# Optimization experiments

Hardware: AMD Instinct MI355X
Metric: run time of the kernel (lower is better)

The kernel has to match this reference:

```python
import jax, jax.numpy as jnp
from jax import lax
import numpy as np

B, L, D, HS, T, N = 1024, 96, 128, 512, 24, 128  # batch, former_seq_len, input_dim, hidden_dim, output_dim, temp_node


def setup_inputs() -> dict:
    key = jax.random.key(0)
    ks = jax.random.split(key, 14)
    s = 1.0 / np.sqrt(HS)  # init std used by the torch module
    f32 = jnp.float32
    return {
        "H": jax.random.normal(ks[0], (B, L, D), f32),
        "y_0": jax.random.normal(ks[1], (B, 1), f32),
        "embedding": jax.random.normal(ks[2], (B, 2 * HS), f32),
        "Y": jax.random.normal(ks[3], (B, T), f32),
        "Wa": jax.random.normal(ks[4], (D, T, N), f32) * s,
        "Ua": jax.random.normal(ks[5], (HS, T, N), f32) * s,
        "ba": jax.random.normal(ks[6], (T, N), f32) * s,
        "Va": jax.random.normal(ks[7], (N, T, 1), f32) * s,
        "W": jax.random.normal(ks[8], (D, T, 4 * HS), f32) * s,
        "U": jax.random.normal(ks[9], (HS, T, 4 * HS), f32) * s,
        "bias": jax.random.normal(ks[10], (T, 4 * HS), f32) * s,
        "W_y": jax.random.normal(ks[11], (1, T, 4 * HS), f32) * s,
        "fc_w": jax.random.normal(ks[12], (T, HS), f32) * s,  # output_fc[t].weight (row vec)
        "fc_b": jax.random.normal(ks[13], (T,), f32) * s,      # output_fc[t].bias
        "epoch": 3,
    }


def reference(H, y_0, embedding, Y, Wa, Ua, ba, Va, W, U, bias, W_y, fc_w, fc_b, epoch):
    scale = 1.0 / jnp.sqrt(jnp.asarray(HS, H.dtype))
    h0 = embedding[:, :HS]
    c0 = embedding[:, HS:]

    # time-major parameter stacks for lax.scan
    xs = (
        jnp.transpose(Wa, (1, 0, 2)),   # [T, D, N]
        jnp.transpose(Ua, (1, 0, 2)),   # [T, HS, N]
        ba,                              # [T, N]
        jnp.transpose(Va, (1, 0, 2)),   # [T, N, 1]
        jnp.transpose(W, (1, 0, 2)),    # [T, D, 4HS]
        jnp.transpose(U, (1, 0, 2)),    # [T, HS, 4HS]
        bias,                            # [T, 4HS]
        jnp.transpose(W_y, (1, 0, 2)),  # [T, 1, 4HS]
        fc_w,                            # [T, HS]
        fc_b,                            # [T]
    )

    def step(carry, p):
        h_l, c_l, y_prev = carry  # [B,HS], [B,HS], [B,1]
        wa, ua, ba_t, va, w, u, b, wy, fw, fb = p
        # temporal attention over the encoder history
        e = jnp.tanh(jnp.einsum('bld,dn->bln', H, wa) + (c_l @ ua)[:, None, :] + ba_t)  # [B,L,N]
        score = jnp.einsum('bln,n->bl', e, va[:, 0]) * scale                              # [B,L]
        beta = jax.nn.softmax(score, axis=1)
        h_t = jnp.einsum('bl,bld->bd', beta, H)                                           # [B,D]
        # 4-gate LSTM update with teacher-signal injection
        gates = h_t @ w + h_l @ u + b + y_prev @ wy                                       # [B,4HS]
        i = jax.nn.sigmoid(gates[:, :HS])
        f = jax.nn.sigmoid(gates[:, HS:2 * HS])
        g = jnp.tanh(gates[:, 2 * HS:3 * HS])
        o = jax.nn.sigmoid(gates[:, 3 * HS:])
        c_new = f * c_l + i * g
        h_new = o * jnp.tanh(c_new)
        y = h_new @ fw + fb                                                               # [B]
        return (h_new, c_new, y[:, None]), (y, h_new)

    _, (ys, hs) = lax.scan(step, (h0, c0, y_0), xs)
    y_out = ys.T                           # [B, T]
    hidden_seq = jnp.transpose(hs, (1, 0, 2))  # [B, T, HS]
    return y_out, hidden_seq
```

## Files before the change

kernel.cpp:

```cpp
#include <hip/hip_runtime.h>
#include <math.h>

constexpr int NB  = 1024;
constexpr int NL  = 96;
constexpr int ND  = 128;
constexpr int NHS = 512;
constexpr int NT  = 24;
constexpr int NN  = 128;
constexpr int NG4 = 4 * NHS;
constexpr int NK  = ND + NHS;
constexpr int BL  = NB * NL;

typedef __attribute__((ext_vector_type(8))) short bf16x8;
typedef __attribute__((ext_vector_type(4))) float f32x4;

static __device__ __forceinline__ unsigned short f2b(float x) {
    union { float f; unsigned u; } v; v.f = x;
    unsigned r = v.u + 0x7fffu + ((v.u >> 16) & 1u);
    return (unsigned short)(r >> 16);
}
static __device__ __forceinline__ float b2f(unsigned short s) {
    union { unsigned u; float f; } v; v.u = ((unsigned)s) << 16;
    return v.f;
}

constexpr float LOG2E  = 1.4426950408889634f;
static __device__ __forceinline__ float fast_exp(float x) {
    return __builtin_amdgcn_exp2f(x * LOG2E);
}
static __device__ __forceinline__ float fast_tanh(float x) {
    float e2 = __builtin_amdgcn_exp2f(x * (2.0f * LOG2E));
    return 1.0f - 2.0f * __builtin_amdgcn_rcpf(1.0f + e2);
}
static __device__ __forceinline__ float fast_sigmoid(float x) {
    float e = __builtin_amdgcn_exp2f(-x * LOG2E);
    return __builtin_amdgcn_rcpf(1.0f + e);
}

__global__ __launch_bounds__(256) void k_init(const float* __restrict__ emb,
                                              const float* __restrict__ y0,
                                              float* __restrict__ c,
                                              unsigned short* __restrict__ Ab0,
                                              float* __restrict__ y) {
    int idx = blockIdx.x * blockDim.x + threadIdx.x;
    if (idx < NB * NHS) {
        int b = idx / NHS, s = idx - b * NHS;
        Ab0[(size_t)b * NK + ND + s] = f2b(emb[b * 2 * NHS + s]);
        c[idx] = emb[b * 2 * NHS + NHS + s];
    }
    if (idx < NB) y[idx] = y0[idx];
}

__global__ __launch_bounds__(256) void k_prep(const float* __restrict__ H,
                                              unsigned short* __restrict__ Hbf) {
    int idx = (blockIdx.x * 256 + threadIdx.x) * 8;
    float4 a = *(const float4*)(H + idx);
    float4 b = *(const float4*)(H + idx + 4);
    bf16x8 o;
    o[0] = (short)f2b(a.x); o[1] = (short)f2b(a.y);
    o[2] = (short)f2b(a.z); o[3] = (short)f2b(a.w);
    o[4] = (short)f2b(b.x); o[5] = (short)f2b(b.y);
    o[6] = (short)f2b(b.z); o[7] = (short)f2b(b.w);
    *(bf16x8*)(Hbf + idx) = o;
}

__global__ __launch_bounds__(128) void k_prepwa(const float* __restrict__ Wa,
                                                unsigned short* __restrict__ Wab) {
    int tn = blockIdx.x;
    int t = tn / NN, n = tn - t * NN;
    int d = threadIdx.x;
    Wab[(size_t)tn * ND + d] = f2b(Wa[(size_t)d * (NT * NN) + t * NN + n]);
}

__global__ __launch_bounds__(256) void k_prepw(const float* __restrict__ W,
                                               const float* __restrict__ U,
                                               unsigned short* __restrict__ Wg) {
    __shared__ unsigned short ts[64][66];
    int nc = blockIdx.x;
    int kc = blockIdx.y;
    int t  = blockIdx.z;
    int tid = threadIdx.x;
    int rowt = tid >> 4;
    int n4   = (tid & 15) << 2;
#pragma unroll
    for (int i = 0; i < 4; ++i) {
        int kl = i * 16 + rowt;
        int k  = kc * 64 + kl;
        const float* src = (k < ND) ? (W + (size_t)k * (NT * NG4))
                                    : (U + (size_t)(k - ND) * (NT * NG4));
        float4 v = *(const float4*)&src[t * NG4 + nc * 64 + n4];
        ts[kl][n4 + 0] = f2b(v.x);
        ts[kl][n4 + 1] = f2b(v.y);
        ts[kl][n4 + 2] = f2b(v.z);
        ts[kl][n4 + 3] = f2b(v.w);
    }
    __syncthreads();
    size_t base = (((size_t)t * 10 + kc) * NG4 + nc * 64) * 64;
#pragma unroll
    for (int p = 0; p < 2; ++p) {
        int flat = p * 256 + tid;
        int nl = flat >> 3, k8 = (flat & 7) << 3;
        bf16x8 o;
#pragma unroll
        for (int j = 0; j < 8; ++j) o[j] = (short)ts[k8 + j][nl];
        *(bf16x8*)&Wg[base + (size_t)nl * 64 + k8] = o;
    }
}

__global__ __launch_bounds__(256) void k_cua0(const float* __restrict__ c,
                                              const float* __restrict__ Ua,
                                              float* __restrict__ cua_part) {
    __shared__ float cs[16][132];
    int m0 = blockIdx.x * 16, n0 = blockIdx.y;
    int tid = threadIdx.x;
#pragma unroll
    for (int i = 0; i < 8; ++i) {
        int idx = tid + i * 256;
        int row = idx >> 7, k = idx & 127;
        cs[row][k] = c[(size_t)(m0 + row) * NHS + n0 * 128 + k];
    }
    __syncthreads();
    int n = tid & 127, rg = tid >> 7;
    float a8[8] = {0, 0, 0, 0, 0, 0, 0, 0};
    for (int k = 0; k < 128; ++k) {
        float ua = Ua[(size_t)(n0 * 128 + k) * (NT * NN) + n];
#pragma unroll
        for (int i = 0; i < 8; ++i) a8[i] += cs[rg * 8 + i][k] * ua;
    }
#pragma unroll
    for (int i = 0; i < 8; ++i)
        cua_part[((size_t)(m0 + rg * 8 + i) * 4 + n0) * 128 + n] = a8[i];
}

__global__ __launch_bounds__(384, 2) void k_attn_fused(
        const unsigned short* __restrict__ Hbf,
        const unsigned short* __restrict__ Wab,
        const float* __restrict__ Va,
        const float* __restrict__ ba,
        const float* __restrict__ cua_part,
        const float* __restrict__ fcb,
        const float* __restrict__ y_part,
        float* __restrict__ y_st,
        float* __restrict__ out_y,
        unsigned short* __restrict__ Ab,
        int t) {
    __shared__ unsigned short Ws[NN][136];
    __shared__ float sc[NL];
    __shared__ float cua_s[NN];
    __shared__ float red[24][ND];
    int tid = threadIdx.x;
    int b = blockIdx.x;

    const unsigned short* src = Wab + (size_t)t * NN * ND;
    for (int f = tid; f < 2048; f += 384) {
        int n = f >> 4, d0 = (f & 15) << 3;
        *(bf16x8*)&Ws[n][d0] = *(const bf16x8*)(src + n * ND + d0);
    }
    if (tid < 128) {
        const float* cp = cua_part + (size_t)b * 4 * 128 + tid;
        cua_s[tid] = cp[0] + cp[128] + cp[256] + cp[384] + ba[t * NN + tid];
    }
    if (t > 0 && tid == 383) {
        const float* yp = y_part + b * 4;
        float yv = fcb[t - 1] + yp[0] + yp[1] + yp[2] + yp[3];
        y_st[b] = yv;
        out_y[b * NT + (t - 1)] = yv;
    }
    __syncthreads();

    int lane = tid & 63, wave = tid >> 6;
    int ln = lane & 15, kg = lane >> 4;
    const unsigned short* Hrow = Hbf + ((size_t)b * NL + wave * 16 + ln) * ND;

    f32x4 zero = {0.f, 0.f, 0.f, 0.f};
    f32x4 acc[8];
#pragma unroll
    for (int nt = 0; nt < 8; ++nt) acc[nt] = zero;
#pragma unroll
    for (int kc = 0; kc < 4; ++kc) {
        int d0 = kc * 32 + kg * 8;
        bf16x8 a = *(const bf16x8*)(Hrow + d0);
#pragma unroll
        for (int nt = 0; nt < 8; ++nt) {
            bf16x8 bb = *(const bf16x8*)&Ws[nt * 16 + ln][d0];
            acc[nt] = __builtin_amdgcn_mfma_f32_16x16x32_bf16(a, bb, acc[nt], 0, 0, 0);
        }
    }
    float va_l[8];
#pragma unroll
    for (int nt = 0; nt < 8; ++nt) va_l[nt] = Va[(nt * 16 + ln) * NT + t];
    const float scale = 0.044194173824159216f;
#pragma unroll
    for (int r = 0; r < 4; ++r) {
        float s = 0.f;
#pragma unroll
        for (int nt = 0; nt < 8; ++nt) {
            float pre = acc[nt][r] + cua_s[nt * 16 + ln];
            s += va_l[nt] * fast_tanh(pre);
        }
#pragma unroll
        for (int off = 1; off < 16; off <<= 1) s += __shfl_xor(s, off);
        if (ln == 0) sc[wave * 16 + kg * 4 + r] = s * scale;
    }
    __syncthreads();

    if (tid < 64) {
        float s0 = sc[tid];
        float s1 = (tid < 32) ? sc[64 + tid] : -1e30f;
        float m = fmaxf(s0, s1);
#pragma unroll
        for (int off = 32; off; off >>= 1) m = fmaxf(m, __shfl_xor(m, off));
        float p0 = fast_exp(s0 - m);
        float p1 = (tid < 32) ? fast_exp(s1 - m) : 0.f;
        float ssum = p0 + p1;
#pragma unroll
        for (int off = 32; off; off >>= 1) ssum += __shfl_xor(ssum, off);
        float inv = __builtin_amdgcn_rcpf(ssum);
        sc[tid] = p0 * inv;
        if (tid < 32) sc[64 + tid] = p1 * inv;
    }
    __syncthreads();

    int dc = tid & 15, lg = tid >> 4;
    int d0 = dc * 8;
    const unsigned short* Hb = Hbf + (size_t)b * NL * ND;
    float a8[8] = {0, 0, 0, 0, 0, 0, 0, 0};
#pragma unroll
    for (int i = 0; i < 4; ++i) {
        int l = lg * 4 + i;
        bf16x8 hv = *(const bf16x8*)(Hb + l * ND + d0);
        float w = sc[l];
#pragma unroll
        for (int j = 0; j < 8; ++j) a8[j] += w * b2f((unsigned short)hv[j]);
    }
#pragma unroll
    for (int j = 0; j < 8; ++j) red[lg][d0 + j] = a8[j];
    __syncthreads();
    if (tid < ND) {
        float accd = 0.f;
#pragma unroll
        for (int g = 0; g < 24; ++g) accd += red[g][tid];
        Ab[(size_t)b * NK + tid] = f2b(accd);
    }
}

__global__ __launch_bounds__(256, 2) void k_gates_cell(
        const unsigned short* __restrict__ Ab,
        unsigned short* __restrict__ AbN,
        const unsigned short* __restrict__ Wg,
        const float* __restrict__ bias,
        const float* __restrict__ Wy,
        const float* __restrict__ fcw,
        const float* __restrict__ Ua,
        const float* __restrict__ y_st,
        float* __restrict__ c,
        float* __restrict__ out_h,
        float* __restrict__ y_part,
        float* __restrict__ cua_part,
        int t) {
    __shared__ __align__(16) char pool[73728];
    __shared__ float ys[16];
    __shared__ float yredL[16][2];
    int tid = threadIdx.x;
    int lane = tid & 63, wave = tid >> 6;
    int ln = lane & 15, kg = lane >> 4;
    int m0 = blockIdx.x * 16, n0 = blockIdx.y;

    if (tid < 16) ys[tid] = y_st[m0 + tid];

    unsigned short* BstW = (unsigned short*)pool + wave * (128 * 72);
    const unsigned short* Arow = Ab + (size_t)(m0 + ln) * NK;

    f32x4 zero = {0.f, 0.f, 0.f, 0.f};
    f32x4 acc[8];
#pragma unroll
    for (int nt = 0; nt < 8; ++nt) acc[nt] = zero;

    for (int kb = 0; kb < 10; ++kb) {
        const unsigned short* Wkb = Wg
            + (((size_t)(t * 10 + kb)) * NG4 + wave * NHS + n0 * 128) * 64;
#pragma unroll
        for (int i = 0; i < 16; ++i) {
            int flat = i * 64 + lane;
            int n = flat >> 3, k8 = (flat & 7) << 3;
            *(bf16x8*)&BstW[n * 72 + k8] = *(const bf16x8*)(Wkb + (size_t)n * 64 + k8);
        }
#pragma unroll
        for (int kc = 0; kc < 2; ++kc) {
            int d0 = kc * 32 + kg * 8;
            bf16x8 a = *(const bf16x8*)(Arow + kb * 64 + d0);
#pragma unroll
            for (int nt = 0; nt < 8; ++nt) {
                bf16x8 bb = *(const bf16x8*)&BstW[(nt * 16 + ln) * 72 + d0];
                acc[nt] = __builtin_amdgcn_mfma_f32_16x16x32_bf16(a, bb, acc[nt], 0, 0, 0);
            }
        }
    }
    __syncthreads();

    float* gs = (float*)pool;
    float* cs = (float*)(pool + 33792);
#pragma unroll
    for (int nt = 0; nt < 8; ++nt)
#pragma unroll
        for (int r = 0; r < 4; ++r)
            gs[wave * 2112 + (kg * 4 + r) * 132 + nt * 16 + ln] = acc[nt][r];
    __syncthreads();

    int s_loc = tid & 127, rg = tid >> 7;
    int s_glob = n0 * 128 + s_loc;
    float prow[8];
#pragma unroll
    for (int i = 0; i < 8; ++i) {
        int row = rg * 8 + i;
        int b = m0 + row;
        float yp = ys[row];
        float gi = gs[0 * 2112 + row * 132 + s_loc] + bias[t * NG4 + s_glob]
                 + yp * Wy[t * NG4 + s_glob];
        float gf = gs[1 * 2112 + row * 132 + s_loc] + bias[t * NG4 + NHS + s_glob]
                 + yp * Wy[t * NG4 + NHS + s_glob];
        float gg = gs[2 * 2112 + row * 132 + s_loc] + bias[t * NG4 + 2 * NHS + s_glob]
                 + yp * Wy[t * NG4 + 2 * NHS + s_glob];
        float go = gs[3 * 2112 + row * 132 + s_loc] + bias[t * NG4 + 3 * NHS + s_glob]
                 + yp * Wy[t * NG4 + 3 * NHS + s_glob];
        float iv = fast_sigmoid(gi);
        float fv = fast_sigmoid(gf);
        float gv = fast_tanh(gg);
        float ov = fast_sigmoid(go);
        float cn = fv * c[(size_t)b * NHS + s_glob] + iv * gv;
        float hn = ov * fast_tanh(cn);
        c[(size_t)b * NHS + s_glob] = cn;
        cs[row * 132 + s_loc] = cn;
        AbN[(size_t)b * NK + ND + s_glob] = f2b(hn);
        out_h[(size_t)b * (NT * NHS) + t * NHS + s_glob] = hn;
        prow[i] = hn * fcw[t * NHS + s_glob];
    }
#pragma unroll
    for (int i = 0; i < 8; ++i) {
        float v = prow[i];
#pragma unroll
        for (int off = 32; off; off >>= 1) v += __shfl_xor(v, off);
        if (lane == 0) yredL[rg * 8 + i][(tid >> 6) & 1] = v;
    }
    __syncthreads();
    if (tid < 16)
        y_part[(size_t)(m0 + tid) * 4 + n0] = yredL[tid][0] + yredL[tid][1];

    if (t + 1 < NT) {
        float a8[8] = {0, 0, 0, 0, 0, 0, 0, 0};
        int n = s_loc;
        for (int k = 0; k < 128; ++k) {
            float ua = Ua[(size_t)(n0 * 128 + k) * (NT * NN) + (t + 1) * NN + n];
#pragma unroll
            for (int i = 0; i < 8; ++i) a8[i] += cs[(rg * 8 + i) * 132 + k] * ua;
        }
#pragma unroll
        for (int i = 0; i < 8; ++i)
            cua_part[((size_t)(m0 + rg * 8 + i) * 4 + n0) * 128 + n] = a8[i];
    }
}

__global__ __launch_bounds__(256) void k_yfin(const float* __restrict__ y_part,
                                              const float* __restrict__ fcb,
                                              float* __restrict__ out_y) {
    int b = blockIdx.x * 256 + threadIdx.x;
    if (b < NB) {
        const float* yp = y_part + (size_t)b * 4;
        out_y[b * NT + (NT - 1)] = fcb[NT - 1] + yp[0] + yp[1] + yp[2] + yp[3];
    }
}

extern "C" void kernel_launch(void* const* d_in, const int* in_sizes, int n_in,
                              void* d_out, int out_size, void* d_ws, size_t ws_size,
                              hipStream_t stream) {
    (void)in_sizes; (void)n_in; (void)out_size; (void)ws_size;
    const float* H    = (const float*)d_in[0];
    const float* y0   = (const float*)d_in[1];
    const float* emb  = (const float*)d_in[2];
    const float* Wa   = (const float*)d_in[4];
    const float* Ua   = (const float*)d_in[5];
    const float* ba   = (const float*)d_in[6];
    const float* Va   = (const float*)d_in[7];
    const float* W    = (const float*)d_in[8];
    const float* U    = (const float*)d_in[9];
    const float* bias = (const float*)d_in[10];
    const float* Wy   = (const float*)d_in[11];
    const float* fcw  = (const float*)d_in[12];
    const float* fcb  = (const float*)d_in[13];

    float* out_y = (float*)d_out;
    float* out_h = out_y + NB * NT;

    float* ws       = (float*)d_ws;
    float* c_st     = ws;
    float* y_st     = c_st + NB * NHS;
    float* y_part   = y_st + NB;
    float* cua_part = y_part + NB * 4;
    unsigned short* Hbf = (unsigned short*)(cua_part + NB * 4 * 128);
    unsigned short* Wab = Hbf + (size_t)BL * ND;
    unsigned short* Ab0 = Wab + (size_t)NT * NN * ND;
    unsigned short* Ab1 = Ab0 + (size_t)NB * NK;
    unsigned short* Wg  = Ab1 + (size_t)NB * NK;

    hipLaunchKernelGGL(k_init, dim3((NB * NHS) / 256), dim3(256), 0, stream,
                       emb, y0, c_st, Ab0, y_st);
    hipLaunchKernelGGL(k_prep, dim3(BL * ND / (256 * 8)), dim3(256), 0, stream, H, Hbf);
    hipLaunchKernelGGL(k_prepwa, dim3(NT * NN), dim3(128), 0, stream, Wa, Wab);
    hipLaunchKernelGGL(k_prepw, dim3(32, 10, 24), dim3(256), 0, stream, W, U, Wg);
    hipLaunchKernelGGL(k_cua0, dim3(64, 4), dim3(256), 0, stream, c_st, Ua, cua_part);

    for (int t = 0; t < NT; ++t) {
        unsigned short* Ab  = (t & 1) ? Ab1 : Ab0;
        unsigned short* AbN = (t & 1) ? Ab0 : Ab1;
        hipLaunchKernelGGL(k_attn_fused, dim3(NB), dim3(384), 0, stream,
                           Hbf, Wab, Va, ba, cua_part, fcb, y_part, y_st, out_y, Ab, t);
        hipLaunchKernelGGL(k_gates_cell, dim3(64, 4), dim3(256), 0, stream,
                           Ab, AbN, Wg, bias, Wy, fcw, Ua, y_st, c_st,
                           out_h, y_part, cua_part, t);
    }
    hipLaunchKernelGGL(k_yfin, dim3(NB / 256), dim3(256), 0, stream, y_part, fcb, out_y);
}
```

Before: 1.365 ms.

## Fuse per-timestep attention and LSTM kernels into one persistent cooperative kernel

Replaces the 48 per-timestep kernel launches (attention plus gates/cell) and the final y kernel with a single cooperative persistent kernel of 256 blocks × 512 threads that loops over timesteps and uses grid-wide syncs between phases. Each block now handles 4 batch rows for attention and a 16×128 gate tile. The aim is to remove launch overhead and inter-kernel gaps. In exchange it adds grid barrier cost, lowers parallelism (256 blocks versus 1024 for attention), and changes the weighted-sum loop to a scalar per-element form.

```diff
diff --git a/kernel.cpp b/kernel.cpp
--- a/kernel.cpp
+++ b/kernel.cpp
@@ -1,5 +1,8 @@
 #include <hip/hip_runtime.h>
+#include <hip/hip_cooperative_groups.h>
 #include <math.h>
+
+namespace cg = cooperative_groups;
 
 constexpr int NB  = 1024;
 constexpr int NL  = 96;
@@ -132,239 +135,234 @@
         cua_part[((size_t)(m0 + rg * 8 + i) * 4 + n0) * 128 + n] = a8[i];
 }
 
-__global__ __launch_bounds__(384, 2) void k_attn_fused(
+__global__ __launch_bounds__(512, 2) void k_seq(
         const unsigned short* __restrict__ Hbf,
         const unsigned short* __restrict__ Wab,
         const float* __restrict__ Va,
         const float* __restrict__ ba,
-        const float* __restrict__ cua_part,
-        const float* __restrict__ fcb,
-        const float* __restrict__ y_part,
-        float* __restrict__ y_st,
-        float* __restrict__ out_y,
-        unsigned short* __restrict__ Ab,
-        int t) {
-    __shared__ unsigned short Ws[NN][136];
-    __shared__ float sc[NL];
-    __shared__ float cua_s[NN];
-    __shared__ float red[24][ND];
-    int tid = threadIdx.x;
-    int b = blockIdx.x;
-
-    const unsigned short* src = Wab + (size_t)t * NN * ND;
-    for (int f = tid; f < 2048; f += 384) {
-        int n = f >> 4, d0 = (f & 15) << 3;
-        *(bf16x8*)&Ws[n][d0] = *(const bf16x8*)(src + n * ND + d0);
-    }
-    if (tid < 128) {
-        const float* cp = cua_part + (size_t)b * 4 * 128 + tid;
-        cua_s[tid] = cp[0] + cp[128] + cp[256] + cp[384] + ba[t * NN + tid];
-    }
-    if (t > 0 && tid == 383) {
-        const float* yp = y_part + b * 4;
-        float yv = fcb[t - 1] + yp[0] + yp[1] + yp[2] + yp[3];
-        y_st[b] = yv;
-        out_y[b * NT + (t - 1)] = yv;
-    }
-    __syncthreads();
-
-    int lane = tid & 63, wave = tid >> 6;
-    int ln = lane & 15, kg = lane >> 4;
-    const unsigned short* Hrow = Hbf + ((size_t)b * NL + wave * 16 + ln) * ND;
-
-    f32x4 zero = {0.f, 0.f, 0.f, 0.f};
-    f32x4 acc[8];
-#pragma unroll
-    for (int nt = 0; nt < 8; ++nt) acc[nt] = zero;
-#pragma unroll
-    for (int kc = 0; kc < 4; ++kc) {
-        int d0 = kc * 32 + kg * 8;
-        bf16x8 a = *(const bf16x8*)(Hrow + d0);
-#pragma unroll
-        for (int nt = 0; nt < 8; ++nt) {
-            bf16x8 bb = *(const bf16x8*)&Ws[nt * 16 + ln][d0];
-            acc[nt] = __builtin_amdgcn_mfma_f32_16x16x32_bf16(a, bb, acc[nt], 0, 0, 0);
-        }
-    }
-    float va_l[8];
-#pragma unroll
-    for (int nt = 0; nt < 8; ++nt) va_l[nt] = Va[(nt * 16 + ln) * NT + t];
-    const float scale = 0.044194173824159216f;
-#pragma unroll
-    for (int r = 0; r < 4; ++r) {
-        float s = 0.f;
-#pragma unroll
-        for (int nt = 0; nt < 8; ++nt) {
-            float pre = acc[nt][r] + cua_s[nt * 16 + ln];
-            s += va_l[nt] * fast_tanh(pre);
-        }
-#pragma unroll
-        for (int off = 1; off < 16; off <<= 1) s += __shfl_xor(s, off);
-        if (ln == 0) sc[wave * 16 + kg * 4 + r] = s * scale;
-    }
-    __syncthreads();
-
-    if (tid < 64) {
-        float s0 = sc[tid];
-        float s1 = (tid < 32) ? sc[64 + tid] : -1e30f;
-        float m = fmaxf(s0, s1);
-#pragma unroll
-        for (int off = 32; off; off >>= 1) m = fmaxf(m, __shfl_xor(m, off));
-        float p0 = fast_exp(s0 - m);
-        float p1 = (tid < 32) ? fast_exp(s1 - m) : 0.f;
-        float ssum = p0 + p1;
-#pragma unroll
-        for (int off = 32; off; off >>= 1) ssum += __shfl_xor(ssum, off);
-        float inv = __builtin_amdgcn_rcpf(ssum);
-        sc[tid] = p0 * inv;
-        if (tid < 32) sc[64 + tid] = p1 * inv;
-    }
-    __syncthreads();
-
-    int dc = tid & 15, lg = tid >> 4;
-    int d0 = dc * 8;
-    const unsigned short* Hb = Hbf + (size_t)b * NL * ND;
-    float a8[8] = {0, 0, 0, 0, 0, 0, 0, 0};
-#pragma unroll
-    for (int i = 0; i < 4; ++i) {
-        int l = lg * 4 + i;
-        bf16x8 hv = *(const bf16x8*)(Hb + l * ND + d0);
-        float w = sc[l];
-#pragma unroll
-        for (int j = 0; j < 8; ++j) a8[j] += w * b2f((unsigned short)hv[j]);
-    }
-#pragma unroll
-    for (int j = 0; j < 8; ++j) red[lg][d0 + j] = a8[j];
-    __syncthreads();
-    if (tid < ND) {
-        float accd = 0.f;
-#pragma unroll
-        for (int g = 0; g < 24; ++g) accd += red[g][tid];
-        Ab[(size_t)b * NK + tid] = f2b(accd);
-    }
-}
-
-__global__ __launch_bounds__(256, 2) void k_gates_cell(
-        const unsigned short* __restrict__ Ab,
-        unsigned short* __restrict__ AbN,
-        const unsigned short* __restrict__ Wg,
         const float* __restrict__ bias,
         const float* __restrict__ Wy,
         const float* __restrict__ fcw,
+        const float* __restrict__ fcb,
         const float* __restrict__ Ua,
-        const float* __restrict__ y_st,
+        const unsigned short* __restrict__ Wg,
         float* __restrict__ c,
-        float* __restrict__ out_h,
+        float* __restrict__ y_st,
         float* __restrict__ y_part,
         float* __restrict__ cua_part,
-        int t) {
+        unsigned short* __restrict__ Ab0,
+        unsigned short* __restrict__ Ab1,
+        float* __restrict__ out_y,
+        float* __restrict__ out_h) {
+    cg::grid_group gg = cg::this_grid();
     __shared__ __align__(16) char pool[73728];
-    __shared__ float ys[16];
+    __shared__ float sc4[4][NL];
+    __shared__ float cua_s4[4][NN];
     __shared__ float yredL[16][2];
+
+    int blk = blockIdx.x;
     int tid = threadIdx.x;
     int lane = tid & 63, wave = tid >> 6;
     int ln = lane & 15, kg = lane >> 4;
-    int m0 = blockIdx.x * 16, n0 = blockIdx.y;
-
-    if (tid < 16) ys[tid] = y_st[m0 + tid];
-
-    unsigned short* BstW = (unsigned short*)pool + wave * (128 * 72);
-    const unsigned short* Arow = Ab + (size_t)(m0 + ln) * NK;
-
+    int b0 = blk * 4;
+    const float scale_c = 0.044194173824159216f;
     f32x4 zero = {0.f, 0.f, 0.f, 0.f};
-    f32x4 acc[8];
-#pragma unroll
-    for (int nt = 0; nt < 8; ++nt) acc[nt] = zero;
-
-    for (int kb = 0; kb < 10; ++kb) {
-        const unsigned short* Wkb = Wg
-            + (((size_t)(t * 10 + kb)) * NG4 + wave * NHS + n0 * 128) * 64;
-#pragma unroll
-        for (int i = 0; i < 16; ++i) {
-            int flat = i * 64 + lane;
-            int n = flat >> 3, k8 = (flat & 7) << 3;
-            *(bf16x8*)&BstW[n * 72 + k8] = *(const bf16x8*)(Wkb + (size_t)n * 64 + k8);
+
+    for (int t = 0; t < NT; ++t) {
+        unsigned short* AbC = (t & 1) ? Ab1 : Ab0;
+        unsigned short* AbN = (t & 1) ? Ab0 : Ab1;
+
+        {
+            unsigned short* Ws = (unsigned short*)pool;
+            const unsigned short* src = Wab + (size_t)t * NN * ND;
+#pragma unroll
+            for (int f = 0; f < 4; ++f) {
+                int idx = tid + f * 512;
+                int n = idx >> 4, d0 = (idx & 15) << 3;
+                *(bf16x8*)&Ws[n * 136 + d0] = *(const bf16x8*)(src + n * ND + d0);
+            }
+            {
+                int bl = tid >> 7, n = tid & 127;
+                const float* cp = cua_part + (size_t)(b0 + bl) * 512 + n;
+                cua_s4[bl][n] = cp[0] + cp[128] + cp[256] + cp[384] + ba[t * NN + n];
+            }
+            if (t > 0 && tid < 4) {
+                int b = b0 + tid;
+                const float* yp = y_part + (size_t)b * 4;
+                float yv = fcb[t - 1] + yp[0] + yp[1] + yp[2] + yp[3];
+                y_st[b] = yv;
+                out_y[b * NT + (t - 1)] = yv;
+            }
+            __syncthreads();
+
+            float va_l[8];
+#pragma unroll
+            for (int nt = 0; nt < 8; ++nt) va_l[nt] = Va[(nt * 16 + ln) * NT + t];
+
+#pragma unroll
+            for (int ti = 0; ti < 3; ++ti) {
+                int tau = wave + ti * 8;
+                int bl = tau / 6, r0 = (tau % 6) * 16;
+                const unsigned short* Hrow = Hbf + ((size_t)(b0 + bl) * NL + r0 + ln) * ND;
+                f32x4 acc[8];
+#pragma unroll
+                for (int nt = 0; nt < 8; ++nt) acc[nt] = zero;
+#pragma unroll
+                for (int kc = 0; kc < 4; ++kc) {
+                    int d0 = kc * 32 + kg * 8;
+                    bf16x8 a = *(const bf16x8*)(Hrow + d0);
+#pragma unroll
+                    for (int nt = 0; nt < 8; ++nt) {
+                        bf16x8 bb = *(const bf16x8*)&Ws[(nt * 16 + ln) * 136 + d0];
+                        acc[nt] = __builtin_amdgcn_mfma_f32_16x16x32_bf16(a, bb, acc[nt], 0, 0, 0);
+                    }
+                }
+#pragma unroll
+                for (int r = 0; r < 4; ++r) {
+                    float s = 0.f;
+#pragma unroll
+                    for (int nt = 0; nt < 8; ++nt) {
+                        float pre = acc[nt][r] + cua_s4[bl][nt * 16 + ln];
+                        s += va_l[nt] * fast_tanh(pre);
+                    }
+#pragma unroll
+                    for (int off = 1; off < 16; off <<= 1) s += __shfl_xor(s, off);
+                    if (ln == 0) sc4[bl][r0 + kg * 4 + r] = s * scale_c;
+                }
+            }
+            __syncthreads();
+
+            if (wave < 4) {
+                float s0 = sc4[wave][lane];
+                float s1 = (lane < 32) ? sc4[wave][64 + lane] : -1e30f;
+                float m = fmaxf(s0, s1);
+#pragma unroll
+                for (int off = 32; off; off >>= 1) m = fmaxf(m, __shfl_xor(m, off));
+                float p0 = fast_exp(s0 - m);
+                float p1 = (lane < 32) ? fast_exp(s1 - m) : 0.f;
+                float ssum = p0 + p1;
+#pragma unroll
+                for (int off = 32; off; off >>= 1) ssum += __shfl_xor(ssum, off);
+                float inv = __builtin_amdgcn_rcpf(ssum);
+                sc4[wave][lane] = p0 * inv;
+                if (lane < 32) sc4[wave][64 + lane] = p1 * inv;
+            }
+            __syncthreads();
+
+            {
+                int bl = tid >> 7, dd = tid & 127;
+                const unsigned short* Hb = Hbf + (size_t)(b0 + bl) * NL * ND;
+                float a0 = 0.f;
+                for (int l = 0; l < NL; ++l)
+                    a0 += sc4[bl][l] * b2f(Hb[(size_t)l * ND + dd]);
+                AbC[(size_t)(b0 + bl) * NK + dd] = f2b(a0);
+            }
         }
-#pragma unroll
-        for (int kc = 0; kc < 2; ++kc) {
-            int d0 = kc * 32 + kg * 8;
-            bf16x8 a = *(const bf16x8*)(Arow + kb * 64 + d0);
-#pragma unroll
-            for (int nt = 0; nt < 8; ++nt) {
-                bf16x8 bb = *(const bf16x8*)&BstW[(nt * 16 + ln) * 72 + d0];
-                acc[nt] = __builtin_amdgcn_mfma_f32_16x16x32_bf16(a, bb, acc[nt], 0, 0, 0);
+        gg.sync();
+
+        {
+            int m0 = (blk >> 2) * 16, n0 = blk & 3;
+            int g = wave >> 1, nh = wave & 1;
+            unsigned short* Bst = (unsigned short*)pool;
+            const unsigned short* Arow = AbC + (size_t)(m0 + ln) * NK;
+            f32x4 acc[4];
+#pragma unroll
+            for (int nt = 0; nt < 4; ++nt) acc[nt] = zero;
+
+            for (int kb = 0; kb < 10; ++kb) {
+                const unsigned short* Wkb = Wg +
+                    (((size_t)(t * 10 + kb)) * NG4 + g * NHS + n0 * 128 + nh * 64) * 64;
+                unsigned short* dst = Bst + (size_t)(g * 128 + nh * 64) * 72;
+#pragma unroll
+                for (int i = 0; i < 8; ++i) {
+                    int flat = i * 64 + lane;
+                    int n = flat >> 3, k8 = (flat & 7) << 3;
+                    *(bf16x8*)&dst[n * 72 + k8] = *(const bf16x8*)(Wkb + (size_t)n * 64 + k8);
+                }
+#pragma unroll
+                for (int kc = 0; kc < 2; ++kc) {
+                    int d0 = kc * 32 + kg * 8;
+                    bf16x8 a = *(const bf16x8*)(Arow + kb * 64 + d0);
+#pragma unroll
+                    for (int nt = 0; nt < 4; ++nt) {
+                        bf16x8 bb = *(const bf16x8*)&dst[(nt * 16 + ln) * 72 + d0];
+                        acc[nt] = __builtin_amdgcn_mfma_f32_16x16x32_bf16(a, bb, acc[nt], 0, 0, 0);
+                    }
+                }
+            }
+            __syncthreads();
+
+            float* gs = (float*)pool;
+            float* cs = (float*)(pool + 33792);
+#pragma unroll
+            for (int nt = 0; nt < 4; ++nt)
+#pragma unroll
+                for (int r = 0; r < 4; ++r)
+                    gs[g * 2112 + (kg * 4 + r) * 132 + nh * 64 + nt * 16 + ln] = acc[nt][r];
+            __syncthreads();
+
+            int s_loc = tid & 127, rg4 = tid >> 7;
+            int s_glob = n0 * 128 + s_loc;
+            float bi0 = bias[t * NG4 + s_glob];
+            float bi1 = bias[t * NG4 + NHS + s_glob];
+            float bi2 = bias[t * NG4 + 2 * NHS + s_glob];
+            float bi3 = bias[t * NG4 + 3 * NHS + s_glob];
+            float wy0 = Wy[t * NG4 + s_glob];
+            float wy1 = Wy[t * NG4 + NHS + s_glob];
+            float wy2 = Wy[t * NG4 + 2 * NHS + s_glob];
+            float wy3 = Wy[t * NG4 + 3 * NHS + s_glob];
+            float fw  = fcw[t * NHS + s_glob];
+            float prow[4];
+#pragma unroll
+            for (int i = 0; i < 4; ++i) {
+                int row = rg4 * 4 + i;
+                int b = m0 + row;
+                float yp = y_st[b];
+                float gi  = gs[0 * 2112 + row * 132 + s_loc] + bi0 + yp * wy0;
+                float gf  = gs[1 * 2112 + row * 132 + s_loc] + bi1 + yp * wy1;
+                float gg2 = gs[2 * 2112 + row * 132 + s_loc] + bi2 + yp * wy2;
+                float go  = gs[3 * 2112 + row * 132 + s_loc] + bi3 + yp * wy3;
+                float iv = fast_sigmoid(gi);
+                float fv = fast_sigmoid(gf);
+                float gv = fast_tanh(gg2);
+                float ov = fast_sigmoid(go);
+                float cn = fv * c[(size_t)b * NHS + s_glob] + iv * gv;
+                float hn = ov * fast_tanh(cn);
+                c[(size_t)b * NHS + s_glob] = cn;
+                cs[row * 132 + s_loc] = cn;
+                AbN[(size_t)b * NK + ND + s_glob] = f2b(hn);
+                out_h[(size_t)b * (NT * NHS) + t * NHS + s_glob] = hn;
+                prow[i] = hn * fw;
+            }
+#pragma unroll
+            for (int i = 0; i < 4; ++i) {
+                float v = prow[i];
+#pragma unroll
+                for (int off = 32; off; off >>= 1) v += __shfl_xor(v, off);
+                if (lane == 0) yredL[rg4 * 4 + i][(tid >> 6) & 1] = v;
+            }
+            __syncthreads();
+            if (tid < 16)
+                y_part[(size_t)(m0 + tid) * 4 + n0] = yredL[tid][0] + yredL[tid][1];
+
+            if (t + 1 < NT) {
+                float a4[4] = {0.f, 0.f, 0.f, 0.f};
+                int n = s_loc;
+                for (int k = 0; k < 128; ++k) {
+                    float ua = Ua[(size_t)(n0 * 128 + k) * (NT * NN) + (t + 1) * NN + n];
+#pragma unroll
+                    for (int i = 0; i < 4; ++i) a4[i] += cs[(rg4 * 4 + i) * 132 + k] * ua;
+                }
+#pragma unroll
+                for (int i = 0; i < 4; ++i)
+                    cua_part[((size_t)(m0 + rg4 * 4 + i) * 4 + n0) * 128 + n] = a4[i];
             }
         }
-    }
-    __syncthreads();
-
-    float* gs = (float*)pool;
-    float* cs = (float*)(pool + 33792);
-#pragma unroll
-    for (int nt = 0; nt < 8; ++nt)
-#pragma unroll
-        for (int r = 0; r < 4; ++r)
-            gs[wave * 2112 + (kg * 4 + r) * 132 + nt * 16 + ln] = acc[nt][r];
-    __syncthreads();
-
-    int s_loc = tid & 127, rg = tid >> 7;
-    int s_glob = n0 * 128 + s_loc;
-    float prow[8];
-#pragma unroll
-    for (int i = 0; i < 8; ++i) {
-        int row = rg * 8 + i;
-        int b = m0 + row;
-        float yp = ys[row];
-        float gi = gs[0 * 2112 + row * 132 + s_loc] + bias[t * NG4 + s_glob]
-                 + yp * Wy[t * NG4 + s_glob];
-        float gf = gs[1 * 2112 + row * 132 + s_loc] + bias[t * NG4 + NHS + s_glob]
-                 + yp * Wy[t * NG4 + NHS + s_glob];
-        float gg = gs[2 * 2112 + row * 132 + s_loc] + bias[t * NG4 + 2 * NHS + s_glob]
-                 + yp * Wy[t * NG4 + 2 * NHS + s_glob];
-        float go = gs[3 * 2112 + row * 132 + s_loc] + bias[t * NG4 + 3 * NHS + s_glob]
-                 + yp * Wy[t * NG4 + 3 * NHS + s_glob];
-        float iv = fast_sigmoid(gi);
-        float fv = fast_sigmoid(gf);
-        float gv = fast_tanh(gg);
-        float ov = fast_sigmoid(go);
-        float cn = fv * c[(size_t)b * NHS + s_glob] + iv * gv;
-        float hn = ov * fast_tanh(cn);
-        c[(size_t)b * NHS + s_glob] = cn;
-        cs[row * 132 + s_loc] = cn;
-        AbN[(size_t)b * NK + ND + s_glob] = f2b(hn);
-        out_h[(size_t)b * (NT * NHS) + t * NHS + s_glob] = hn;
-        prow[i] = hn * fcw[t * NHS + s_glob];
-    }
-#pragma unroll
-    for (int i = 0; i < 8; ++i) {
-        float v = prow[i];
-#pragma unroll
-        for (int off = 32; off; off >>= 1) v += __shfl_xor(v, off);
-        if (lane == 0) yredL[rg * 8 + i][(tid >> 6) & 1] = v;
-    }
-    __syncthreads();
-    if (tid < 16)
-        y_part[(size_t)(m0 + tid) * 4 + n0] = yredL[tid][0] + yredL[tid][1];
-
-    if (t + 1 < NT) {
-        float a8[8] = {0, 0, 0, 0, 0, 0, 0, 0};
-        int n = s_loc;
-        for (int k = 0; k < 128; ++k) {
-            float ua = Ua[(size_t)(n0 * 128 + k) * (NT * NN) + (t + 1) * NN + n];
-#pragma unroll
-            for (int i = 0; i < 8; ++i) a8[i] += cs[(rg * 8 + i) * 132 + k] * ua;
-        }
-#pragma unroll
-        for (int i = 0; i < 8; ++i)
-            cua_part[((size_t)(m0 + rg * 8 + i) * 4 + n0) * 128 + n] = a8[i];
-    }
-}
-
-__global__ __launch_bounds__(256) void k_yfin(const float* __restrict__ y_part,
-                                              const float* __restrict__ fcb,
-                                              float* __restrict__ out_y) {
-    int b = blockIdx.x * 256 + threadIdx.x;
-    if (b < NB) {
+        gg.sync();
+    }
+
+    if (tid < 4) {
+        int b = blk * 4 + tid;
         const float* yp = y_part + (size_t)b * 4;
         out_y[b * NT + (NT - 1)] = fcb[NT - 1] + yp[0] + yp[1] + yp[2] + yp[3];
     }
@@ -409,14 +407,12 @@
     hipLaunchKernelGGL(k_prepw, dim3(32, 10, 24), dim3(256), 0, stream, W, U, Wg);
     hipLaunchKernelGGL(k_cua0, dim3(64, 4), dim3(256), 0, stream, c_st, Ua, cua_part);
 
-    for (int t = 0; t < NT; ++t) {
-        unsigned short* Ab  = (t & 1) ? Ab1 : Ab0;
-        unsigned short* AbN = (t & 1) ? Ab0 : Ab1;
-        hipLaunchKernelGGL(k_attn_fused, dim3(NB), dim3(384), 0, stream,
-                           Hbf, Wab, Va, ba, cua_part, fcb, y_part, y_st, out_y, Ab, t);
-        hipLaunchKernelGGL(k_gates_cell, dim3(64, 4), dim3(256), 0, stream,
-                           Ab, AbN, Wg, bias, Wy, fcw, Ua, y_st, c_st,
-                           out_h, y_part, cua_part, t);
-    }
-    hipLaunchKernelGGL(k_yfin, dim3(NB / 256), dim3(256), 0, stream, y_part, fcb, out_y);
-}
+    void* args[] = {
+        (void*)&Hbf, (void*)&Wab, (void*)&Va, (void*)&ba, (void*)&bias,
+        (void*)&Wy, (void*)&fcw, (void*)&fcb, (void*)&Ua, (void*)&Wg,
+        (void*)&c_st, (void*)&y_st, (void*)&y_part, (void*)&cua_part,
+        (void*)&Ab0, (void*)&Ab1, (void*)&out_y, (void*)&out_h
+    };
+    hipLaunchCooperativeKernel(reinterpret_cast<void*>(k_seq),
+                               dim3(256), dim3(512), args, 0, stream);
+}
```

After: 3.786 ms. 177% more time.

## Retile gates-cell kernel to 32x64 blocks with direct global B-fragment loads

Applied to the files above, without the earlier changes.

The LSTM gate kernel now uses 32-row by 64-column blocks with 512 threads and a (32,8) grid. Each wave computes a 2x2 grid of MFMA tiles and reads weight fragments straight from global memory instead of staging them in shared memory. This cuts shared-memory use and doubles reuse of each weight fragment across rows. The hidden dimension is now split into 8 partial sums instead of 4, so the Ua projection, y partials and all their consumers (k_cua0, attention, yfin) are changed to match. The risk is uncached global B loads and more partial-sum traffic in exchange for better occupancy and more blocks.

```diff
diff --git a/kernel.cpp b/kernel.cpp
--- a/kernel.cpp
+++ b/kernel.cpp
@@ -110,26 +110,26 @@
 __global__ __launch_bounds__(256) void k_cua0(const float* __restrict__ c,
                                               const float* __restrict__ Ua,
                                               float* __restrict__ cua_part) {
-    __shared__ float cs[16][132];
+    __shared__ float cs[16][64];
     int m0 = blockIdx.x * 16, n0 = blockIdx.y;
     int tid = threadIdx.x;
 #pragma unroll
-    for (int i = 0; i < 8; ++i) {
+    for (int i = 0; i < 4; ++i) {
         int idx = tid + i * 256;
-        int row = idx >> 7, k = idx & 127;
-        cs[row][k] = c[(size_t)(m0 + row) * NHS + n0 * 128 + k];
-    }
-    __syncthreads();
-    int n = tid & 127, rg = tid >> 7;
+        int row = idx >> 6, k = idx & 63;
+        cs[row][k] = c[(size_t)(m0 + row) * NHS + n0 * 64 + k];
+    }
+    __syncthreads();
+    int n = tid & 127, bg = tid >> 7;
     float a8[8] = {0, 0, 0, 0, 0, 0, 0, 0};
-    for (int k = 0; k < 128; ++k) {
-        float ua = Ua[(size_t)(n0 * 128 + k) * (NT * NN) + n];
-#pragma unroll
-        for (int i = 0; i < 8; ++i) a8[i] += cs[rg * 8 + i][k] * ua;
+    for (int k = 0; k < 64; ++k) {
+        float ua = Ua[(size_t)(n0 * 64 + k) * (NT * NN) + n];
+#pragma unroll
+        for (int i = 0; i < 8; ++i) a8[i] += cs[bg * 8 + i][k] * ua;
     }
 #pragma unroll
     for (int i = 0; i < 8; ++i)
-        cua_part[((size_t)(m0 + rg * 8 + i) * 4 + n0) * 128 + n] = a8[i];
+        cua_part[((size_t)(m0 + bg * 8 + i) * 8 + n0) * 128 + n] = a8[i];
 }
 
 __global__ __launch_bounds__(384, 2) void k_attn_fused(
@@ -157,12 +157,17 @@
         *(bf16x8*)&Ws[n][d0] = *(const bf16x8*)(src + n * ND + d0);
     }
     if (tid < 128) {
-        const float* cp = cua_part + (size_t)b * 4 * 128 + tid;
-        cua_s[tid] = cp[0] + cp[128] + cp[256] + cp[384] + ba[t * NN + tid];
+        const float* cp = cua_part + (size_t)b * 8 * 128 + tid;
+        float s = ba[t * NN + tid];
+#pragma unroll
+        for (int p = 0; p < 8; ++p) s += cp[p * 128];
+        cua_s[tid] = s;
     }
     if (t > 0 && tid == 383) {
-        const float* yp = y_part + b * 4;
-        float yv = fcb[t - 1] + yp[0] + yp[1] + yp[2] + yp[3];
+        const float* yp = y_part + (size_t)b * 8;
+        float yv = fcb[t - 1];
+#pragma unroll
+        for (int p = 0; p < 8; ++p) yv += yp[p];
         y_st[b] = yv;
         out_y[b * NT + (t - 1)] = yv;
     }
@@ -244,7 +249,7 @@
     }
 }
 
-__global__ __launch_bounds__(256, 2) void k_gates_cell(
+__global__ __launch_bounds__(512) void k_gates_cell(
         const unsigned short* __restrict__ Ab,
         unsigned short* __restrict__ AbN,
         const unsigned short* __restrict__ Wg,
@@ -258,105 +263,102 @@
         float* __restrict__ y_part,
         float* __restrict__ cua_part,
         int t) {
-    __shared__ __align__(16) char pool[73728];
-    __shared__ float ys[16];
-    __shared__ float yredL[16][2];
+    __shared__ float gs[4][32][68];
+    __shared__ float cs[32][68];
     int tid = threadIdx.x;
     int lane = tid & 63, wave = tid >> 6;
     int ln = lane & 15, kg = lane >> 4;
-    int m0 = blockIdx.x * 16, n0 = blockIdx.y;
-
-    if (tid < 16) ys[tid] = y_st[m0 + tid];
-
-    unsigned short* BstW = (unsigned short*)pool + wave * (128 * 72);
-    const unsigned short* Arow = Ab + (size_t)(m0 + ln) * NK;
+    int m0 = blockIdx.x * 32, n0 = blockIdx.y;
+    int g = wave >> 1, hf = wave & 1;
+    int cb = g * NHS + n0 * 64 + hf * 32;
+
+    const unsigned short* A0 = Ab + (size_t)(m0 + ln) * NK;
+    const unsigned short* A1 = Ab + (size_t)(m0 + 16 + ln) * NK;
 
     f32x4 zero = {0.f, 0.f, 0.f, 0.f};
-    f32x4 acc[8];
-#pragma unroll
-    for (int nt = 0; nt < 8; ++nt) acc[nt] = zero;
+    f32x4 acc[2][2];
+#pragma unroll
+    for (int rt = 0; rt < 2; ++rt)
+#pragma unroll
+        for (int nt = 0; nt < 2; ++nt) acc[rt][nt] = zero;
 
     for (int kb = 0; kb < 10; ++kb) {
-        const unsigned short* Wkb = Wg
-            + (((size_t)(t * 10 + kb)) * NG4 + wave * NHS + n0 * 128) * 64;
-#pragma unroll
-        for (int i = 0; i < 16; ++i) {
-            int flat = i * 64 + lane;
-            int n = flat >> 3, k8 = (flat & 7) << 3;
-            *(bf16x8*)&BstW[n * 72 + k8] = *(const bf16x8*)(Wkb + (size_t)n * 64 + k8);
-        }
+        const unsigned short* Wkb = Wg + ((size_t)(t * 10 + kb) * NG4) * 64;
 #pragma unroll
         for (int kc = 0; kc < 2; ++kc) {
             int d0 = kc * 32 + kg * 8;
-            bf16x8 a = *(const bf16x8*)(Arow + kb * 64 + d0);
-#pragma unroll
-            for (int nt = 0; nt < 8; ++nt) {
-                bf16x8 bb = *(const bf16x8*)&BstW[(nt * 16 + ln) * 72 + d0];
-                acc[nt] = __builtin_amdgcn_mfma_f32_16x16x32_bf16(a, bb, acc[nt], 0, 0, 0);
+            bf16x8 a0 = *(const bf16x8*)(A0 + kb * 64 + d0);
+            bf16x8 a1 = *(const bf16x8*)(A1 + kb * 64 + d0);
+#pragma unroll
+            for (int nt = 0; nt < 2; ++nt) {
+                bf16x8 bb = *(const bf16x8*)(Wkb + (size_t)(cb + nt * 16 + ln) * 64 + d0);
+                acc[0][nt] = __builtin_amdgcn_mfma_f32_16x16x32_bf16(a0, bb, acc[0][nt], 0, 0, 0);
+                acc[1][nt] = __builtin_amdgcn_mfma_f32_16x16x32_bf16(a1, bb, acc[1][nt], 0, 0, 0);
             }
         }
     }
-    __syncthreads();
-
-    float* gs = (float*)pool;
-    float* cs = (float*)(pool + 33792);
-#pragma unroll
-    for (int nt = 0; nt < 8; ++nt)
-#pragma unroll
-        for (int r = 0; r < 4; ++r)
-            gs[wave * 2112 + (kg * 4 + r) * 132 + nt * 16 + ln] = acc[nt][r];
-    __syncthreads();
-
-    int s_loc = tid & 127, rg = tid >> 7;
-    int s_glob = n0 * 128 + s_loc;
-    float prow[8];
-#pragma unroll
-    for (int i = 0; i < 8; ++i) {
-        int row = rg * 8 + i;
+#pragma unroll
+    for (int rt = 0; rt < 2; ++rt)
+#pragma unroll
+        for (int nt = 0; nt < 2; ++nt)
+#pragma unroll
+            for (int r = 0; r < 4; ++r)
+                gs[g][rt * 16 + kg * 4 + r][hf * 32 + nt * 16 + ln] = acc[rt][nt][r];
+    __syncthreads();
+
+    int s_loc = tid & 63, rg = tid >> 6;
+    int s_glob = n0 * 64 + s_loc;
+    float bi0 = bias[t * NG4 + s_glob];
+    float bi1 = bias[t * NG4 + NHS + s_glob];
+    float bi2 = bias[t * NG4 + 2 * NHS + s_glob];
+    float bi3 = bias[t * NG4 + 3 * NHS + s_glob];
+    float wy0 = Wy[t * NG4 + s_glob];
+    float wy1 = Wy[t * NG4 + NHS + s_glob];
+    float wy2 = Wy[t * NG4 + 2 * NHS + s_glob];
+    float wy3 = Wy[t * NG4 + 3 * NHS + s_glob];
+    float fw  = fcw[t * NHS + s_glob];
+    float prow[4];
+#pragma unroll
+    for (int i = 0; i < 4; ++i) {
+        int row = rg * 4 + i;
         int b = m0 + row;
-        float yp = ys[row];
-        float gi = gs[0 * 2112 + row * 132 + s_loc] + bias[t * NG4 + s_glob]
-                 + yp * Wy[t * NG4 + s_glob];
-        float gf = gs[1 * 2112 + row * 132 + s_loc] + bias[t * NG4 + NHS + s_glob]
-                 + yp * Wy[t * NG4 + NHS + s_glob];
-        float gg = gs[2 * 2112 + row * 132 + s_loc] + bias[t * NG4 + 2 * NHS + s_glob]
-                 + yp * Wy[t * NG4 + 2 * NHS + s_glob];
-        float go = gs[3 * 2112 + row * 132 + s_loc] + bias[t * NG4 + 3 * NHS + s_glob]
-                 + yp * Wy[t * NG4 + 3 * NHS + s_glob];
+        float yp = y_st[b];
+        float gi  = gs[0][row][s_loc] + bi0 + yp * wy0;
+        float gf  = gs[1][row][s_loc] + bi1 + yp * wy1;
+        float gg2 = gs[2][row][s_loc] + bi2 + yp * wy2;
+        float go  = gs[3][row][s_loc] + bi3 + yp * wy3;
         float iv = fast_sigmoid(gi);
         float fv = fast_sigmoid(gf);
-        float gv = fast_tanh(gg);
+        float gv = fast_tanh(gg2);
         float ov = fast_sigmoid(go);
         float cn = fv * c[(size_t)b * NHS + s_glob] + iv * gv;
         float hn = ov * fast_tanh(cn);
         c[(size_t)b * NHS + s_glob] = cn;
-        cs[row * 132 + s_loc] = cn;
+        cs[row][s_loc] = cn;
         AbN[(size_t)b * NK + ND + s_glob] = f2b(hn);
         out_h[(size_t)b * (NT * NHS) + t * NHS + s_glob] = hn;
-        prow[i] = hn * fcw[t * NHS + s_glob];
-    }
-#pragma unroll
-    for (int i = 0; i < 8; ++i) {
+        prow[i] = hn * fw;
+    }
+#pragma unroll
+    for (int i = 0; i < 4; ++i) {
         float v = prow[i];
 #pragma unroll
         for (int off = 32; off; off >>= 1) v += __shfl_xor(v, off);
-        if (lane == 0) yredL[rg * 8 + i][(tid >> 6) & 1] = v;
-    }
-    __syncthreads();
-    if (tid < 16)
-        y_part[(size_t)(m0 + tid) * 4 + n0] = yredL[tid][0] + yredL[tid][1];
+        if (lane == 0) y_part[(size_t)(m0 + rg * 4 + i) * 8 + n0] = v;
+    }
+    __syncthreads();
 
     if (t + 1 < NT) {
+        int n = tid & 127, bg = tid >> 7;
         float a8[8] = {0, 0, 0, 0, 0, 0, 0, 0};
-        int n = s_loc;
-        for (int k = 0; k < 128; ++k) {
-            float ua = Ua[(size_t)(n0 * 128 + k) * (NT * NN) + (t + 1) * NN + n];
-#pragma unroll
-            for (int i = 0; i < 8; ++i) a8[i] += cs[(rg * 8 + i) * 132 + k] * ua;
+        for (int k = 0; k < 64; ++k) {
+            float ua = Ua[(size_t)(n0 * 64 + k) * (NT * NN) + (t + 1) * NN + n];
+#pragma unroll
+            for (int i = 0; i < 8; ++i) a8[i] += cs[bg * 8 + i][k] * ua;
         }
 #pragma unroll
         for (int i = 0; i < 8; ++i)
-            cua_part[((size_t)(m0 + rg * 8 + i) * 4 + n0) * 128 + n] = a8[i];
+            cua_part[((size_t)(m0 + bg * 8 + i) * 8 + n0) * 128 + n] = a8[i];
     }
 }
 
@@ -365,8 +367,11 @@
                                               float* __restrict__ out_y) {
     int b = blockIdx.x * 256 + threadIdx.x;
     if (b < NB) {
-        const float* yp = y_part + (size_t)b * 4;
-        out_y[b * NT + (NT - 1)] = fcb[NT - 1] + yp[0] + yp[1] + yp[2] + yp[3];
+        const float* yp = y_part + (size_t)b * 8;
+        float yv = fcb[NT - 1];
+#pragma unroll
+        for (int p = 0; p < 8; ++p) yv += yp[p];
+        out_y[b * NT + (NT - 1)] = yv;
     }
 }
 
@@ -395,8 +400,8 @@
     float* c_st     = ws;
     float* y_st     = c_st + NB * NHS;
     float* y_part   = y_st + NB;
-    float* cua_part = y_part + NB * 4;
-    unsigned short* Hbf = (unsigned short*)(cua_part + NB * 4 * 128);
+    float* cua_part = y_part + NB * 8;
+    unsigned short* Hbf = (unsigned short*)(cua_part + NB * 8 * 128);
     unsigned short* Wab = Hbf + (size_t)BL * ND;
     unsigned short* Ab0 = Wab + (size_t)NT * NN * ND;
     unsigned short* Ab1 = Ab0 + (size_t)NB * NK;
@@ -407,14 +412,14 @@
     hipLaunchKernelGGL(k_prep, dim3(BL * ND / (256 * 8)), dim3(256), 0, stream, H, Hbf);
     hipLaunchKernelGGL(k_prepwa, dim3(NT * NN), dim3(128), 0, stream, Wa, Wab);
     hipLaunchKernelGGL(k_prepw, dim3(32, 10, 24), dim3(256), 0, stream, W, U, Wg);
-    hipLaunchKernelGGL(k_cua0, dim3(64, 4), dim3(256), 0, stream, c_st, Ua, cua_part);
+    hipLaunchKernelGGL(k_cua0, dim3(64, 8), dim3(256), 0, stream, c_st, Ua, cua_part);
 
     for (int t = 0; t < NT; ++t) {
         unsigned short* Ab  = (t & 1) ? Ab1 : Ab0;
         unsigned short* AbN = (t & 1) ? Ab0 : Ab1;
         hipLaunchKernelGGL(k_attn_fused, dim3(NB), dim3(384), 0, stream,
                            Hbf, Wab, Va, ba, cua_part, fcb, y_part, y_st, out_y, Ab, t);
-        hipLaunchKernelGGL(k_gates_cell, dim3(64, 4), dim3(256), 0, stream,
+        hipLaunchKernelGGL(k_gates_cell, dim3(32, 8), dim3(512), 0, stream,
                            Ab, AbN, Wg, bias, Wy, fcw, Ua, y_st, c_st,
                            out_h, y_part, cua_part, t);
     }
```

Result: faster. 1.323 ms (median of 2 runs) (-3.1%).
